# Optimization experiments

Hardware: AMD Instinct MI355X
Metric: run time of the kernel (lower is better)

The kernel has to match this reference:

```python
import jax, jax.numpy as jnp
import numpy as np

N, E, FDIM, HID, HEADS, C, L, G = 50000, 800000, 512, 256, 8, 32, 3, 64
EPS = 1e-5


def setup_inputs() -> dict:
    key = jax.random.key(0)
    ks = jax.random.split(key, 16)
    x = jax.random.normal(ks[0], (N, FDIM), dtype=jnp.float32)
    edge_index = jax.random.randint(ks[1], (2, E), 0, N, dtype=jnp.int32)
    batch = jnp.sort(jax.random.randint(ks[2], (N,), 0, G, dtype=jnp.int32))
    s = lambda f: 1.0 / np.sqrt(f)
    return {
        "x": x,
        "edge_index": edge_index,
        "batch": batch,
        "in_w": jax.random.normal(ks[3], (FDIM, HID), jnp.float32) * s(FDIM),
        "in_b": jnp.zeros((HID,), jnp.float32),
        "gat_w": jax.random.normal(ks[4], (L, HID, HID), jnp.float32) * s(HID),
        "att_src": jax.random.normal(ks[5], (L, HEADS, C), jnp.float32) * s(C),
        "att_dst": jax.random.normal(ks[6], (L, HEADS, C), jnp.float32) * s(C),
        "gat_b": jnp.zeros((L, HID), jnp.float32),
        "res_w": jax.random.normal(ks[7], (L, HID, HID), jnp.float32) * s(HID),
        "res_b": jnp.zeros((L, HID), jnp.float32),
        "ln_g": jnp.ones((L, HID), jnp.float32),
        "ln_b": jnp.zeros((L, HID), jnp.float32),
        "pool_w": jax.random.normal(ks[8], (2 * HID, HID), jnp.float32) * s(2 * HID),
        "pool_b": jnp.zeros((HID,), jnp.float32),
    }


def _gat_layer(h, src, dst, w, a_src, a_dst, b):
    # PyG GATConv, concat=True, negative_slope=0.2, dropout inactive (eval)
    xh = (h @ w).reshape(N, HEADS, C)                      # [N,H,C]
    asn = jnp.einsum('nhc,hc->nh', xh, a_src)              # [N,H]
    adn = jnp.einsum('nhc,hc->nh', xh, a_dst)
    e = jax.nn.leaky_relu(asn[src] + adn[dst], 0.2)        # [E2,H]
    # scatter-softmax over destination neighborhoods
    m = jax.ops.segment_max(e, dst, num_segments=N)
    m = jnp.where(jnp.isfinite(m), m, 0.0)
    ex = jnp.exp(e - m[dst])
    den = jax.ops.segment_sum(ex, dst, num_segments=N)
    alpha = ex / (den[dst] + 1e-16)                        # [E2,H]
    msg = xh[src] * alpha[:, :, None]                      # [E2,H,C]
    out = jax.ops.segment_sum(msg, dst, num_segments=N)    # [N,H,C]
    return out.reshape(N, HID) + b


def _layer_norm(h, g, b):
    mu = jnp.mean(h, axis=-1, keepdims=True)
    var = jnp.mean((h - mu) ** 2, axis=-1, keepdims=True)
    return (h - mu) * jax.lax.rsqrt(var + EPS) * g + b


def reference(x, edge_index, batch, in_w, in_b, gat_w, att_src, att_dst, gat_b,
              res_w, res_b, ln_g, ln_b, pool_w, pool_b):
    loops = jnp.arange(N, dtype=edge_index.dtype)          # GATConv add_self_loops=True
    src = jnp.concatenate([edge_index[0], loops])
    dst = jnp.concatenate([edge_index[1], loops])
    h = x @ in_w + in_b
    for i in range(L):
        h_res = h @ res_w[i] + res_b[i]
        h = _gat_layer(h, src, dst, gat_w[i], att_src[i], att_dst[i], gat_b[i])
        h = jax.nn.relu(_layer_norm(h + h_res, ln_g[i], ln_b[i]))
    ones = jnp.ones((N,), h.dtype)
    cnt = jax.ops.segment_sum(ones, batch, num_segments=G)
    h_mean = jax.ops.segment_sum(h, batch, num_segments=G) / jnp.maximum(cnt, 1.0)[:, None]
    h_max = jax.ops.segment_max(h, batch, num_segments=G)
    h_cat = jnp.concatenate([h_mean, h_max], axis=1)       # [G, 2*HID]
    return jax.nn.relu(h_cat @ pool_w + pool_b)            # [G, HID]
```

## Files before the change

### kernel.cpp

```cpp
#include <hip/hip_runtime.h>
#include <math.h>

#define N_NODES 50000
#define E_EDGES 800000
#define E2 (E_EDGES + N_NODES)
#define M_PAD 50048
#define NBM 391
#define GEMM_BLOCKS 1568
#define FDIM 512
#define HID 256
#define HEADS 8
#define CDIM 32
#define LAYERS 3
#define GRAPHS 64
#define LN_EPS 1e-5f
#define POOL_P 16

typedef unsigned short ushort_t;
typedef __attribute__((ext_vector_type(8))) short short8v;
typedef __attribute__((ext_vector_type(4))) float f32x4;

__device__ __forceinline__ float bf2f(ushort_t u) {
    union { unsigned int i; float f; } v;
    v.i = ((unsigned int)u) << 16;
    return v.f;
}
__device__ __forceinline__ ushort_t f2bf(float f) {
    union { float f; unsigned int u; } v;
    v.f = f;
    unsigned int r = (v.u + 0x7FFFu + ((v.u >> 16) & 1u)) >> 16;
    return (ushort_t)r;
}
__device__ __forceinline__ void gload_lds16(const void* g, void* l) {
    __builtin_amdgcn_global_load_lds(
        (const __attribute__((address_space(1))) void*)g,
        (__attribute__((address_space(3))) void*)l, 16, 0, 0);
}

__global__ void k_count(const int* __restrict__ ei, int* __restrict__ cnt) {
    int e = blockIdx.x * 256 + threadIdx.x;
    if (e >= E2) return;
    int dst = (e < E_EDGES) ? ei[E_EDGES + e] : (e - E_EDGES);
    atomicAdd(&cnt[dst], 1);
}

__global__ void k_scan1(const int* __restrict__ cnt, int* __restrict__ part) {
    __shared__ int s[256];
    int t = threadIdx.x;
    int i = blockIdx.x * 256 + t;
    s[t] = (i < N_NODES) ? cnt[i] : 0;
    __syncthreads();
    for (int d = 128; d > 0; d >>= 1) {
        if (t < d) s[t] += s[t + d];
        __syncthreads();
    }
    if (t == 0) part[blockIdx.x] = s[0];
}

__global__ void k_scan2(int* __restrict__ part, int nb, int* __restrict__ rowptr) {
    __shared__ int s[256];
    int t = threadIdx.x;
    int v = (t < nb) ? part[t] : 0;
    s[t] = v;
    __syncthreads();
    for (int d = 1; d < 256; d <<= 1) {
        int x = (t >= d) ? s[t - d] : 0;
        __syncthreads();
        s[t] += x;
        __syncthreads();
    }
    if (t < nb) part[t] = s[t] - v;
    if (t == 255) rowptr[N_NODES] = s[255];
}

__global__ void k_scan3(const int* __restrict__ cnt, const int* __restrict__ part,
                        int* __restrict__ rowptr) {
    __shared__ int s[256];
    int t = threadIdx.x;
    int i = blockIdx.x * 256 + t;
    int v = (i < N_NODES) ? cnt[i] : 0;
    s[t] = v;
    __syncthreads();
    for (int d = 1; d < 256; d <<= 1) {
        int x = (t >= d) ? s[t - d] : 0;
        __syncthreads();
        s[t] += x;
        __syncthreads();
    }
    if (i < N_NODES) rowptr[i] = part[blockIdx.x] + s[t] - v;
}

__global__ void k_fill(const int* __restrict__ ei, const int* __restrict__ rowptr,
                       int* __restrict__ fill, int* __restrict__ colv) {
    int e = blockIdx.x * 256 + threadIdx.x;
    if (e >= E2) return;
    int src, dst;
    if (e < E_EDGES) { src = ei[e]; dst = ei[E_EDGES + e]; }
    else             { src = dst = e - E_EDGES; }
    int pos = atomicAdd(&fill[dst], 1);
    colv[rowptr[dst] + pos] = src;
}

__global__ void k_bounds(const int* __restrict__ batch, int* __restrict__ rowstart) {
    int n = blockIdx.x * 256 + threadIdx.x;
    if (n >= N_NODES) return;
    int b = batch[n];
    int bp = (n == 0) ? -1 : batch[n - 1];
    for (int g = bp + 1; g <= b; ++g) rowstart[g] = n;
    if (n == N_NODES - 1) {
        for (int g = b + 1; g <= GRAPHS; ++g) rowstart[g] = N_NODES;
    }
}

__global__ __launch_bounds__(256) void k_cast_x(const float* __restrict__ x,
                                                ushort_t* __restrict__ xb) {
    long long i8 = ((long long)blockIdx.x * 256 + threadIdx.x) * 8;
    if (i8 >= (long long)M_PAD * FDIM) return;
    int row = (int)(i8 >> 9);
    ushort_t o[8];
    if (row < N_NODES) {
        const float* p = x + i8;
        #pragma unroll
        for (int j = 0; j < 8; ++j) o[j] = f2bf(p[j]);
    } else {
        #pragma unroll
        for (int j = 0; j < 8; ++j) o[j] = 0;
    }
    *(short8v*)(xb + i8) = *(short8v*)o;
}

#define MAT_ELEMS (HID * HID)
#define WT_TOTAL (2 * (LAYERS - 1) * MAT_ELEMS)
__global__ __launch_bounds__(256) void k_wtrans_all(const float* __restrict__ gat_w,
                                                    const float* __restrict__ res_w,
                                                    ushort_t* __restrict__ wt2) {
    int r = blockIdx.x * 256 + threadIdx.x;
    if (r >= WT_TOTAL) return;
    int mat = r >> 16;
    int layer = 1 + (mat >> 1);
    int isgat = mat & 1;
    int within = r & 65535;
    int k = within >> 8, n = within & 255;
    const float* W = (isgat ? gat_w : res_w) + (size_t)layer * MAT_ELEMS;
    wt2[(size_t)layer * 512 * HID + (size_t)(isgat * 256 + n) * HID + k] =
        f2bf(W[within]);
}

__global__ __launch_bounds__(256) void k_wcomb(const float* __restrict__ in_w,
                                               const float* __restrict__ in_b,
                                               const float* __restrict__ res_w0,
                                               const float* __restrict__ gat_w0,
                                               const float* __restrict__ res_b0,
                                               ushort_t* __restrict__ wtC,
                                               float* __restrict__ bC0,
                                               float* __restrict__ bC1) {
    if (blockIdx.x == 512) {
        int n = threadIdx.x;
        float s0 = 0.f, s1 = 0.f;
        for (int k = 0; k < HID; ++k) {
            float ib = in_b[k];
            s0 += ib * res_w0[(size_t)k * HID + n];
            s1 += ib * gat_w0[(size_t)k * HID + n];
        }
        bC0[n] = s0 + res_b0[n];
        bC1[n] = s1;
        return;
    }
    __shared__ float wrow[HID];
    int n = blockIdx.x;
    {
        int k = threadIdx.x;
        float wv = (n < 256) ? res_w0[(size_t)k * HID + n]
                             : gat_w0[(size_t)k * HID + (n - 256)];
        wrow[k] = bf2f(f2bf(wv));
    }
    __syncthreads();
    #pragma unroll
    for (int h = 0; h < 2; ++h) {
        int f = h * 256 + threadIdx.x;
        const float* irow = in_w + (size_t)f * HID;
        float s = 0.f;
        #pragma unroll 4
        for (int k = 0; k < HID; k += 4) {
            float4 iv = *(const float4*)(irow + k);
            s += iv.x * wrow[k] + iv.y * wrow[k + 1]
               + iv.z * wrow[k + 2] + iv.w * wrow[k + 3];
        }
        wtC[(size_t)n * FDIM + f] = f2bf(s);
    }
}

template<int K>
__global__ __launch_bounds__(512) void k_gemm_bf16(const ushort_t* __restrict__ A,
                                                   const ushort_t* __restrict__ BT,
                                                   const float* __restrict__ bias0,
                                                   const float* __restrict__ bias1,
                                                   ushort_t* __restrict__ C0,
                                                   ushort_t* __restrict__ C1,
                                                   const float* __restrict__ a_src,
                                                   const float* __restrict__ a_dst,
                                                   float* __restrict__ asn,
                                                   float* __restrict__ adn, int M) {
    const int L = blockIdx.x;
    const int chunk = L >> 5, wrd = L & 31;
    const int bmi = chunk * 8 + (wrd & 7);
    if (bmi >= NBM) return;
    const int bm = bmi * 128;
    const int bn = (wrd >> 3) * 128;

    __shared__ char lds[16384] __attribute__((aligned(16)));
    const int t = threadIdx.x, w = t >> 6, l = t & 63;
    const int wr = w & 3, wc = w >> 2;

    const int arow = t >> 2;
    const int aslot = (t & 3) ^ ((arow >> 1) & 3);
    const ushort_t* pa = A + (size_t)(bm + arow) * K + aslot * 8;
    const ushort_t* pb = BT + (size_t)(bn + arow) * K + aslot * 8;
    char* la = lds + w * 1024;
    char* lb = lds + 8192 + w * 1024;

    int aoff[2], boff[4];
    const int kb = l >> 4;
    #pragma unroll
    for (int mi = 0; mi < 2; ++mi) {
        int r = wr * 32 + mi * 16 + (l & 15);
        aoff[mi] = r * 64 + ((kb ^ ((r >> 1) & 3)) << 4);
    }
    #pragma unroll
    for (int ni = 0; ni < 4; ++ni) {
        int c = wc * 64 + ni * 16 + (l & 15);
        boff[ni] = 8192 + c * 64 + ((kb ^ ((c >> 1) & 3)) << 4);
    }

    f32x4 acc[2][4] = {};
    for (int k0 = 0; k0 < K; k0 += 32) {
        gload_lds16(pa + k0, la);
        gload_lds16(pb + k0, lb);
        __syncthreads();
        short8v a[2], b[4];
        #pragma unroll
        for (int mi = 0; mi < 2; ++mi) a[mi] = *(const short8v*)(lds + aoff[mi]);
        #pragma unroll
        for (int ni = 0; ni < 4; ++ni) b[ni] = *(const short8v*)(lds + boff[ni]);
        #pragma unroll
        for (int mi = 0; mi < 2; ++mi)
            #pragma unroll
            for (int ni = 0; ni < 4; ++ni)
                acc[mi][ni] = __builtin_amdgcn_mfma_f32_16x16x32_bf16(
                    a[mi], b[ni], acc[mi][ni], 0, 0, 0);
        __syncthreads();
    }

    ushort_t* C = (bn < 256) ? C0 : C1;
    const float* bias = (bn < 256) ? bias0 : bias1;
    const int cb = (bn < 256) ? bn : bn - 256;
    #pragma unroll
    for (int mi = 0; mi < 2; ++mi) {
        int row = bm + wr * 32 + mi * 16 + (l >> 4) * 4;
        #pragma unroll
        for (int ni = 0; ni < 4; ++ni) {
            int col = cb + wc * 64 + ni * 16 + (l & 15);
            float bv = bias ? bias[col] : 0.f;
            #pragma unroll
            for (int r = 0; r < 4; ++r) {
                if (row + r < M)
                    C[(size_t)(row + r) * HID + col] = f2bf(acc[mi][ni][r] + bv);
            }
        }
    }

    if (asn && bn >= 256) {
        const int cbase = bn - 256;
        #pragma unroll
        for (int mi = 0; mi < 2; ++mi) {
            int row = bm + wr * 32 + mi * 16 + (l >> 4) * 4;
            #pragma unroll
            for (int p = 0; p < 2; ++p) {
                int c0 = cbase + wc * 64 + (2 * p) * 16 + (l & 15);
                int c1c = c0 + 16;
                int head = c0 >> 5;
                float b1a = bias1 ? bias1[c0] : 0.f;
                float b1b = bias1 ? bias1[c1c] : 0.f;
                float as0 = a_src[c0], as1 = a_src[c1c];
                float ad0 = a_dst[c0], ad1 = a_dst[c1c];
                float vs[4], vd[4];
                #pragma unroll
                for (int r = 0; r < 4; ++r) {
                    float x0 = acc[mi][2 * p][r] + b1a;
                    float x1 = acc[mi][2 * p + 1][r] + b1b;
                    vs[r] = x0 * as0 + x1 * as1;
                    vd[r] = x0 * ad0 + x1 * ad1;
                }
                #pragma unroll
                for (int d = 1; d < 16; d <<= 1) {
                    #pragma unroll
                    for (int r = 0; r < 4; ++r) {
                        vs[r] += __shfl_xor(vs[r], d);
                        vd[r] += __shfl_xor(vd[r], d);
                    }
                }
                if ((l & 15) == 0) {
                    #pragma unroll
                    for (int r = 0; r < 4; ++r) {
                        if (row + r < N_NODES) {
                            asn[(row + r) * HEADS + head] = vs[r];
                            adn[(row + r) * HEADS + head] = vd[r];
                        }
                    }
                }
            }
        }
    }
}

__global__ __launch_bounds__(256) void k_agg_ln(const ushort_t* __restrict__ xhb,
                                                const float* __restrict__ asn,
                                                const float* __restrict__ adn,
                                                const int* __restrict__ rowptr,
                                                const int* __restrict__ colv,
                                                const ushort_t* __restrict__ hresb,
                                                const float* __restrict__ gb,
                                                const float* __restrict__ g,
                                                const float* __restrict__ b,
                                                ushort_t* __restrict__ hb) {
    const int wave = threadIdx.x >> 6, lane = threadIdx.x & 63;
    const int n = blockIdx.x * 4 + wave;
    if (n >= N_NODES) return;
    const int half = lane >> 5;
    const int lh = lane & 31;
    const int head = lh >> 2;
    const int ch0 = lh * 8;
    const float adn_h = adn[n * HEADS + head];
    const int j0 = rowptr[n], j1 = rowptr[n + 1];

    float acc[8] = {};
    float den = 0.f;
    int base = j0;
    for (; base + 8 <= j1; base += 8) {
        int idx[4];
        #pragma unroll
        for (int q = 0; q < 4; ++q) idx[q] = colv[base + 2 * q + half];
        short8v u[4];
        #pragma unroll
        for (int q = 0; q < 4; ++q)
            u[q] = *(const short8v*)(xhb + (size_t)idx[q] * HID + ch0);
        float p[4];
        #pragma unroll
        for (int q = 0; q < 4; ++q) {
            float e = asn[idx[q] * HEADS + head] + adn_h;
            e = (e > 0.f) ? e : 0.2f * e;
            p[q] = __expf(e);
        }
        #pragma unroll
        for (int q = 0; q < 4; ++q) {
            den += p[q];
            #pragma unroll
            for (int c = 0; c < 8; ++c)
                acc[c] += p[q] * bf2f((ushort_t)u[q][c]);
        }
    }
    for (; base < j1; base += 2) {
        bool valid = (base + half) < j1;
        int s = valid ? colv[base + half] : n;
        short8v u = *(const short8v*)(xhb + (size_t)s * HID + ch0);
        float e = asn[s * HEADS + head] + adn_h;
        e = (e > 0.f) ? e : 0.2f * e;
        float p = valid ? __expf(e) : 0.f;
        den += p;
        #pragma unroll
        for (int c = 0; c < 8; ++c)
            acc[c] += p * bf2f((ushort_t)u[c]);
    }
    den += __shfl_xor(den, 32);
    #pragma unroll
    for (int c = 0; c < 8; ++c) acc[c] += __shfl_xor(acc[c], 32);

    const float inv = 1.f / (den + 1e-16f);
    short8v hr = *(const short8v*)(hresb + (size_t)n * HID + ch0);
    float4 gbA = *(const float4*)(gb + ch0);
    float4 gbB = *(const float4*)(gb + ch0 + 4);
    float v[8];
    #pragma unroll
    for (int c = 0; c < 8; ++c) {
        float gbv = (c < 4) ? ((const float*)&gbA)[c] : ((const float*)&gbB)[c - 4];
        v[c] = acc[c] * inv + bf2f((ushort_t)hr[c]) + gbv;
    }
    float s = 0.f;
    #pragma unroll
    for (int c = 0; c < 8; ++c) s += v[c];
    #pragma unroll
    for (int d = 1; d < 32; d <<= 1) s += __shfl_xor(s, d);
    const float mu = s * (1.f / HID);
    float q = 0.f;
    #pragma unroll
    for (int c = 0; c < 8; ++c) {
        v[c] -= mu;
        q += v[c] * v[c];
    }
    #pragma unroll
    for (int d = 1; d < 32; d <<= 1) q += __shfl_xor(q, d);
    const float rstd = rsqrtf(q * (1.f / HID) + LN_EPS);
    float4 gA = *(const float4*)(g + ch0);
    float4 gB = *(const float4*)(g + ch0 + 4);
    float4 bA = *(const float4*)(b + ch0);
    float4 bB = *(const float4*)(b + ch0 + 4);
    ushort_t o[8];
    #pragma unroll
    for (int c = 0; c < 8; ++c) {
        float gv = (c < 4) ? ((const float*)&gA)[c] : ((const float*)&gB)[c - 4];
        float bv = (c < 4) ? ((const float*)&bA)[c] : ((const float*)&bB)[c - 4];
        o[c] = f2bf(fmaxf(v[c] * rstd * gv + bv, 0.f));
    }
    if (half == 0)
        *(short8v*)(hb + (size_t)n * HID + ch0) = *(short8v*)o;
}

__global__ __launch_bounds__(256) void k_pool1(const ushort_t* __restrict__ hb,
                                               const int* __restrict__ rowstart,
                                               float* __restrict__ part) {
    int g = blockIdx.x, p = blockIdx.y, c = threadIdx.x;
    int s0 = rowstart[g], s1 = rowstart[g + 1];
    float sum = 0.f, mx = -INFINITY;
    for (int n = s0 + p; n < s1; n += POOL_P) {
        float v = bf2f(hb[(size_t)n * HID + c]);
        sum += v;
        mx = fmaxf(mx, v);
    }
    float* pp = part + (size_t)(g * POOL_P + p) * 512;
    pp[c] = sum;
    pp[256 + c] = mx;
}

__global__ __launch_bounds__(256) void k_pool2g(const float* __restrict__ part,
                                                const int* __restrict__ rowstart,
                                                const float* __restrict__ W,
                                                const float* __restrict__ bias,
                                                float* __restrict__ out) {
    __shared__ float hc[512];
    int g = blockIdx.x, c = threadIdx.x;
    float sum = 0.f, mx = -INFINITY;
    for (int p = 0; p < POOL_P; ++p) {
        const float* pp = part + (size_t)(g * POOL_P + p) * 512;
        sum += pp[c];
        mx = fmaxf(mx, pp[256 + c]);
    }
    float cntf = (float)(rowstart[g + 1] - rowstart[g]);
    hc[c] = sum / fmaxf(cntf, 1.f);
    hc[256 + c] = mx;
    __syncthreads();
    float acc = bias[c];
    #pragma unroll 8
    for (int k = 0; k < 2 * HID; ++k)
        acc += hc[k] * W[(size_t)k * HID + c];
    out[(size_t)g * HID + c] = fmaxf(acc, 0.f);
}

extern "C" void kernel_launch(void* const* d_in, const int* in_sizes, int n_in,
                              void* d_out, int out_size, void* d_ws, size_t ws_size,
                              hipStream_t stream) {
    const float* x       = (const float*)d_in[0];
    const int*   ei      = (const int*)d_in[1];
    const int*   batch   = (const int*)d_in[2];
    const float* in_w    = (const float*)d_in[3];
    const float* in_b    = (const float*)d_in[4];
    const float* gat_w   = (const float*)d_in[5];
    const float* att_src = (const float*)d_in[6];
    const float* att_dst = (const float*)d_in[7];
    const float* gat_b   = (const float*)d_in[8];
    const float* res_w   = (const float*)d_in[9];
    const float* res_b   = (const float*)d_in[10];
    const float* ln_g    = (const float*)d_in[11];
    const float* ln_b    = (const float*)d_in[12];
    const float* pool_w  = (const float*)d_in[13];
    const float* pool_b  = (const float*)d_in[14];
    float* out = (float*)d_out;

    char* ws = (char*)d_ws;
    size_t off = 0;
    auto alloc = [&](size_t bytes) -> char* {
        char* p = ws + off;
        off = (off + bytes + 255) & ~(size_t)255;
        return p;
    };
    ushort_t* xb    = (ushort_t*)alloc((size_t)M_PAD * FDIM * 2);
    ushort_t* hb    = (ushort_t*)alloc((size_t)M_PAD * HID * 2);
    ushort_t* xhb   = (ushort_t*)alloc((size_t)M_PAD * HID * 2);
    ushort_t* hresb = (ushort_t*)alloc((size_t)M_PAD * HID * 2);
    float* asn      = (float*)alloc((size_t)N_NODES * HEADS * 4);
    float* adn      = (float*)alloc((size_t)N_NODES * HEADS * 4);
    int*   cnt      = (int*)alloc((size_t)N_NODES * 4);
    int*   fill     = (int*)alloc((size_t)N_NODES * 4);
    int*   rowptr   = (int*)alloc((size_t)(N_NODES + 1) * 4);
    int*   colv     = (int*)alloc((size_t)E2 * 4);
    int*   part     = (int*)alloc(256 * 4);
    int*   rowstart = (int*)alloc((size_t)(GRAPHS + 1) * 4);
    ushort_t* wt2   = (ushort_t*)alloc((size_t)LAYERS * 512 * HID * 2);
    ushort_t* wtC   = (ushort_t*)alloc((size_t)512 * FDIM * 2);
    float* bC0      = (float*)alloc(HID * 4);
    float* bC1      = (float*)alloc(HID * 4);
    float* poolpart = (float*)alloc((size_t)GRAPHS * POOL_P * 512 * 4);

    hipMemsetAsync(cnt, 0, (size_t)N_NODES * 4, stream);
    hipMemsetAsync(fill, 0, (size_t)N_NODES * 4, stream);

    const int ge = (E2 + 255) / 256;
    const int nb = (N_NODES + 255) / 256;
    k_count<<<ge, 256, 0, stream>>>(ei, cnt);
    k_scan1<<<nb, 256, 0, stream>>>(cnt, part);
    k_scan2<<<1, 256, 0, stream>>>(part, nb, rowptr);
    k_scan3<<<nb, 256, 0, stream>>>(cnt, part, rowptr);
    k_fill<<<ge, 256, 0, stream>>>(ei, rowptr, fill, colv);
    k_bounds<<<nb, 256, 0, stream>>>(batch, rowstart);

    k_cast_x<<<(int)(((size_t)M_PAD * FDIM / 8 + 255) / 256), 256, 0, stream>>>(x, xb);
    k_wtrans_all<<<(WT_TOTAL + 255) / 256, 256, 0, stream>>>(gat_w, res_w, wt2);
    k_wcomb<<<513, 256, 0, stream>>>(in_w, in_b, res_w, gat_w, res_b,
                                     wtC, bC0, bC1);

    const int nw = (N_NODES + 3) / 4;

    k_gemm_bf16<FDIM><<<GEMM_BLOCKS, 512, 0, stream>>>(xb, wtC, bC0, bC1,
                                                       hresb, xhb, att_src, att_dst,
                                                       asn, adn, N_NODES);
    k_agg_ln<<<nw, 256, 0, stream>>>(xhb, asn, adn, rowptr, colv, hresb,
                                     gat_b, ln_g, ln_b, hb);

    for (int i = 1; i < LAYERS; ++i) {
        k_gemm_bf16<HID><<<GEMM_BLOCKS, 512, 0, stream>>>(
            hb, wt2 + (size_t)i * 512 * HID,
            res_b + (size_t)i * HID, nullptr, hresb, xhb,
            att_src + (size_t)i * HEADS * CDIM,
            att_dst + (size_t)i * HEADS * CDIM, asn, adn, N_NODES);
        k_agg_ln<<<nw, 256, 0, stream>>>(xhb, asn, adn, rowptr, colv, hresb,
                                         gat_b + (size_t)i * HID,
                                         ln_g + (size_t)i * HID,
                                         ln_b + (size_t)i * HID, hb);
    }
    dim3 pg(GRAPHS, POOL_P);
    k_pool1<<<pg, 256, 0, stream>>>(hb, rowstart, poolpart);
    k_pool2g<<<GRAPHS, 256, 0, stream>>>(poolpart, rowstart, pool_w, pool_b, out);
}
```

Measured before the change: 570.3 us.

## Fuse fp32-to-bf16 cast of x into first GEMM and merge prep kernels

Removes the separate x cast kernel and its bf16 buffer. The first GEMM now loads fp32 rows of x straight into LDS, using a doubled A tile with an XOR swizzle, and converts them to bf16 in registers with v_cvt_pk_bf16_f32. The edge count, batch bounds, weight transpose and combined-weight kernels are merged into a single k_prep launch, which cuts launch overhead. In exchange the first GEMM reads twice the A bytes and uses more LDS per block, and out-of-range rows are clamped to row 0.

```diff
diff --git a/kernel.cpp b/kernel.cpp
--- a/kernel.cpp
+++ b/kernel.cpp
@@ -37,13 +37,6 @@
         (__attribute__((address_space(3))) void*)l, 16, 0, 0);
 }
 
-__global__ void k_count(const int* __restrict__ ei, int* __restrict__ cnt) {
-    int e = blockIdx.x * 256 + threadIdx.x;
-    if (e >= E2) return;
-    int dst = (e < E_EDGES) ? ei[E_EDGES + e] : (e - E_EDGES);
-    atomicAdd(&cnt[dst], 1);
-}
-
 __global__ void k_scan1(const int* __restrict__ cnt, int* __restrict__ part) {
     __shared__ int s[256];
     int t = threadIdx.x;
@@ -101,60 +94,63 @@
     colv[rowptr[dst] + pos] = src;
 }
 
-__global__ void k_bounds(const int* __restrict__ batch, int* __restrict__ rowstart) {
-    int n = blockIdx.x * 256 + threadIdx.x;
-    if (n >= N_NODES) return;
-    int b = batch[n];
-    int bp = (n == 0) ? -1 : batch[n - 1];
-    for (int g = bp + 1; g <= b; ++g) rowstart[g] = n;
-    if (n == N_NODES - 1) {
-        for (int g = b + 1; g <= GRAPHS; ++g) rowstart[g] = N_NODES;
-    }
-}
-
-__global__ __launch_bounds__(256) void k_cast_x(const float* __restrict__ x,
-                                                ushort_t* __restrict__ xb) {
-    long long i8 = ((long long)blockIdx.x * 256 + threadIdx.x) * 8;
-    if (i8 >= (long long)M_PAD * FDIM) return;
-    int row = (int)(i8 >> 9);
-    ushort_t o[8];
-    if (row < N_NODES) {
-        const float* p = x + i8;
-        #pragma unroll
-        for (int j = 0; j < 8; ++j) o[j] = f2bf(p[j]);
-    } else {
-        #pragma unroll
-        for (int j = 0; j < 8; ++j) o[j] = 0;
-    }
-    *(short8v*)(xb + i8) = *(short8v*)o;
-}
-
+#define GE_BLK ((E2 + 255) / 256)
+#define NB_BLK ((N_NODES + 255) / 256)
 #define MAT_ELEMS (HID * HID)
 #define WT_TOTAL (2 * (LAYERS - 1) * MAT_ELEMS)
-__global__ __launch_bounds__(256) void k_wtrans_all(const float* __restrict__ gat_w,
-                                                    const float* __restrict__ res_w,
-                                                    ushort_t* __restrict__ wt2) {
-    int r = blockIdx.x * 256 + threadIdx.x;
-    if (r >= WT_TOTAL) return;
-    int mat = r >> 16;
-    int layer = 1 + (mat >> 1);
-    int isgat = mat & 1;
-    int within = r & 65535;
-    int k = within >> 8, n = within & 255;
-    const float* W = (isgat ? gat_w : res_w) + (size_t)layer * MAT_ELEMS;
-    wt2[(size_t)layer * 512 * HID + (size_t)(isgat * 256 + n) * HID + k] =
-        f2bf(W[within]);
-}
-
-__global__ __launch_bounds__(256) void k_wcomb(const float* __restrict__ in_w,
-                                               const float* __restrict__ in_b,
-                                               const float* __restrict__ res_w0,
-                                               const float* __restrict__ gat_w0,
-                                               const float* __restrict__ res_b0,
-                                               ushort_t* __restrict__ wtC,
-                                               float* __restrict__ bC0,
-                                               float* __restrict__ bC1) {
-    if (blockIdx.x == 512) {
+#define WT_BLK (WT_TOTAL / 256)
+#define PREP_BLOCKS (GE_BLK + NB_BLK + WT_BLK + 513)
+
+__global__ __launch_bounds__(256) void k_prep(const int* __restrict__ ei,
+                                              const int* __restrict__ batch,
+                                              const float* __restrict__ in_w,
+                                              const float* __restrict__ in_b,
+                                              const float* __restrict__ gat_w,
+                                              const float* __restrict__ res_w,
+                                              const float* __restrict__ res_b,
+                                              int* __restrict__ cnt,
+                                              int* __restrict__ rowstart,
+                                              ushort_t* __restrict__ wt2,
+                                              ushort_t* __restrict__ wtC,
+                                              float* __restrict__ bC0,
+                                              float* __restrict__ bC1) {
+    int bid = blockIdx.x;
+    if (bid < GE_BLK) {
+        int e = bid * 256 + threadIdx.x;
+        if (e >= E2) return;
+        int dst = (e < E_EDGES) ? ei[E_EDGES + e] : (e - E_EDGES);
+        atomicAdd(&cnt[dst], 1);
+        return;
+    }
+    bid -= GE_BLK;
+    if (bid < NB_BLK) {
+        int n = bid * 256 + threadIdx.x;
+        if (n >= N_NODES) return;
+        int b = batch[n];
+        int bp = (n == 0) ? -1 : batch[n - 1];
+        for (int g = bp + 1; g <= b; ++g) rowstart[g] = n;
+        if (n == N_NODES - 1) {
+            for (int g = b + 1; g <= GRAPHS; ++g) rowstart[g] = N_NODES;
+        }
+        return;
+    }
+    bid -= NB_BLK;
+    if (bid < WT_BLK) {
+        int r = bid * 256 + threadIdx.x;
+        int mat = r >> 16;
+        int layer = 1 + (mat >> 1);
+        int isgat = mat & 1;
+        int within = r & 65535;
+        int k = within >> 8, n = within & 255;
+        const float* W = (isgat ? gat_w : res_w) + (size_t)layer * MAT_ELEMS;
+        wt2[(size_t)layer * 512 * HID + (size_t)(isgat * 256 + n) * HID + k] =
+            f2bf(W[within]);
+        return;
+    }
+    bid -= WT_BLK;
+    const float* res_w0 = res_w;
+    const float* gat_w0 = gat_w;
+    if (bid == 512) {
         int n = threadIdx.x;
         float s0 = 0.f, s1 = 0.f;
         for (int k = 0; k < HID; ++k) {
@@ -162,12 +158,12 @@
             s0 += ib * res_w0[(size_t)k * HID + n];
             s1 += ib * gat_w0[(size_t)k * HID + n];
         }
-        bC0[n] = s0 + res_b0[n];
+        bC0[n] = s0 + res_b[n];
         bC1[n] = s1;
         return;
     }
     __shared__ float wrow[HID];
-    int n = blockIdx.x;
+    int n = bid;
     {
         int k = threadIdx.x;
         float wv = (n < 256) ? res_w0[(size_t)k * HID + n]
@@ -190,8 +186,8 @@
     }
 }
 
-template<int K>
-__global__ __launch_bounds__(512) void k_gemm_bf16(const ushort_t* __restrict__ A,
+template<int K, bool AFP32>
+__global__ __launch_bounds__(512) void k_gemm_bf16(const void* __restrict__ Av,
                                                    const ushort_t* __restrict__ BT,
                                                    const float* __restrict__ bias0,
                                                    const float* __restrict__ bias1,
@@ -208,38 +204,78 @@
     const int bm = bmi * 128;
     const int bn = (wrd >> 3) * 128;
 
-    __shared__ char lds[16384] __attribute__((aligned(16)));
+    constexpr int ABYTES = AFP32 ? 16384 : 8192;
+    __shared__ char lds[ABYTES + 8192] __attribute__((aligned(16)));
     const int t = threadIdx.x, w = t >> 6, l = t & 63;
     const int wr = w & 3, wc = w >> 2;
 
-    const int arow = t >> 2;
-    const int aslot = (t & 3) ^ ((arow >> 1) & 3);
-    const ushort_t* pa = A + (size_t)(bm + arow) * K + aslot * 8;
-    const ushort_t* pb = BT + (size_t)(bn + arow) * K + aslot * 8;
-    char* la = lds + w * 1024;
-    char* lb = lds + 8192 + w * 1024;
-
-    int aoff[2], boff[4];
+    const int brow = t >> 2;
+    const int bslot = (t & 3) ^ ((brow >> 1) & 3);
+    const ushort_t* pb = BT + (size_t)(bn + brow) * K + bslot * 8;
+    char* lb = lds + ABYTES + w * 1024;
+
+    const ushort_t* pa = nullptr;
+    const float* paf1 = nullptr;
+    const float* paf2 = nullptr;
+    if constexpr (AFP32) {
+        const int c2 = t + 512;
+        const int ar1 = t >> 3,  as1 = (t & 7) ^ (ar1 & 7);
+        const int ar2 = c2 >> 3, as2 = (c2 & 7) ^ (ar2 & 7);
+        int gr1 = bm + ar1; if (gr1 >= M) gr1 = 0;
+        int gr2 = bm + ar2; if (gr2 >= M) gr2 = 0;
+        paf1 = (const float*)Av + (size_t)gr1 * K + as1 * 4;
+        paf2 = (const float*)Av + (size_t)gr2 * K + as2 * 4;
+    } else {
+        pa = (const ushort_t*)Av + (size_t)(bm + brow) * K + bslot * 8;
+    }
+
     const int kb = l >> 4;
+    int aoff[2];
+    int aoffF[2][2];
+    int boff[4];
     #pragma unroll
     for (int mi = 0; mi < 2; ++mi) {
         int r = wr * 32 + mi * 16 + (l & 15);
-        aoff[mi] = r * 64 + ((kb ^ ((r >> 1) & 3)) << 4);
+        if constexpr (AFP32) {
+            #pragma unroll
+            for (int j = 0; j < 2; ++j)
+                aoffF[mi][j] = r * 128 + (((2 * kb + j) ^ (r & 7)) << 4);
+        } else {
+            aoff[mi] = r * 64 + ((kb ^ ((r >> 1) & 3)) << 4);
+        }
     }
     #pragma unroll
     for (int ni = 0; ni < 4; ++ni) {
         int c = wc * 64 + ni * 16 + (l & 15);
-        boff[ni] = 8192 + c * 64 + ((kb ^ ((c >> 1) & 3)) << 4);
+        boff[ni] = ABYTES + c * 64 + ((kb ^ ((c >> 1) & 3)) << 4);
     }
 
     f32x4 acc[2][4] = {};
     for (int k0 = 0; k0 < K; k0 += 32) {
-        gload_lds16(pa + k0, la);
+        if constexpr (AFP32) {
+            gload_lds16(paf1 + k0, lds + w * 1024);
+            gload_lds16(paf2 + k0, lds + 8192 + w * 1024);
+        } else {
+            gload_lds16(pa + k0, lds + w * 1024);
+        }
         gload_lds16(pb + k0, lb);
         __syncthreads();
         short8v a[2], b[4];
         #pragma unroll
-        for (int mi = 0; mi < 2; ++mi) a[mi] = *(const short8v*)(lds + aoff[mi]);
+        for (int mi = 0; mi < 2; ++mi) {
+            if constexpr (AFP32) {
+                f32x4 f0 = *(const f32x4*)(lds + aoffF[mi][0]);
+                f32x4 f1 = *(const f32x4*)(lds + aoffF[mi][1]);
+                union { unsigned int u[4]; short8v s; } cv;
+                asm("v_cvt_pk_bf16_f32 %0, %1, %2" : "=v"(cv.u[0]) : "v"(f0[0]), "v"(f0[1]));
+                asm("v_cvt_pk_bf16_f32 %0, %1, %2" : "=v"(cv.u[1]) : "v"(f0[2]), "v"(f0[3]));
+                asm("v_cvt_pk_bf16_f32 %0, %1, %2" : "=v"(cv.u[2]) : "v"(f1[0]), "v"(f1[1]));
+                asm("v_cvt_pk_bf16_f32 %0, %1, %2" : "=v"(cv.u[3]) : "v"(f1[2]), "v"(f1[3]));
+                a[mi] = cv.s;
+            } else {
+                a[mi] = *(const short8v*)(lds + aoff[mi]);
+            }
+        }
         #pragma unroll
         for (int ni = 0; ni < 4; ++ni) b[ni] = *(const short8v*)(lds + boff[ni]);
         #pragma unroll
@@ -482,7 +518,6 @@
         off = (off + bytes + 255) & ~(size_t)255;
         return p;
     };
-    ushort_t* xb    = (ushort_t*)alloc((size_t)M_PAD * FDIM * 2);
     ushort_t* hb    = (ushort_t*)alloc((size_t)M_PAD * HID * 2);
     ushort_t* xhb   = (ushort_t*)alloc((size_t)M_PAD * HID * 2);
     ushort_t* hresb = (ushort_t*)alloc((size_t)M_PAD * HID * 2);
@@ -503,31 +538,27 @@
     hipMemsetAsync(cnt, 0, (size_t)N_NODES * 4, stream);
     hipMemsetAsync(fill, 0, (size_t)N_NODES * 4, stream);
 
-    const int ge = (E2 + 255) / 256;
-    const int nb = (N_NODES + 255) / 256;
-    k_count<<<ge, 256, 0, stream>>>(ei, cnt);
+    const int ge = GE_BLK;
+    const int nb = NB_BLK;
+    k_prep<<<PREP_BLOCKS, 256, 0, stream>>>(ei, batch, in_w, in_b, gat_w, res_w,
+                                            res_b, cnt, rowstart, wt2, wtC,
+                                            bC0, bC1);
     k_scan1<<<nb, 256, 0, stream>>>(cnt, part);
     k_scan2<<<1, 256, 0, stream>>>(part, nb, rowptr);
     k_scan3<<<nb, 256, 0, stream>>>(cnt, part, rowptr);
     k_fill<<<ge, 256, 0, stream>>>(ei, rowptr, fill, colv);
-    k_bounds<<<nb, 256, 0, stream>>>(batch, rowstart);
-
-    k_cast_x<<<(int)(((size_t)M_PAD * FDIM / 8 + 255) / 256), 256, 0, stream>>>(x, xb);
-    k_wtrans_all<<<(WT_TOTAL + 255) / 256, 256, 0, stream>>>(gat_w, res_w, wt2);
-    k_wcomb<<<513, 256, 0, stream>>>(in_w, in_b, res_w, gat_w, res_b,
-                                     wtC, bC0, bC1);
 
     const int nw = (N_NODES + 3) / 4;
 
-    k_gemm_bf16<FDIM><<<GEMM_BLOCKS, 512, 0, stream>>>(xb, wtC, bC0, bC1,
-                                                       hresb, xhb, att_src, att_dst,
-                                                       asn, adn, N_NODES);
+    k_gemm_bf16<FDIM, true><<<GEMM_BLOCKS, 512, 0, stream>>>(
+        (const void*)x, wtC, bC0, bC1, hresb, xhb, att_src, att_dst,
+        asn, adn, N_NODES);
     k_agg_ln<<<nw, 256, 0, stream>>>(xhb, asn, adn, rowptr, colv, hresb,
                                      gat_b, ln_g, ln_b, hb);
 
     for (int i = 1; i < LAYERS; ++i) {
-        k_gemm_bf16<HID><<<GEMM_BLOCKS, 512, 0, stream>>>(
-            hb, wt2 + (size_t)i * 512 * HID,
+        k_gemm_bf16<HID, false><<<GEMM_BLOCKS, 512, 0, stream>>>(
+            (const void*)hb, wt2 + (size_t)i * 512 * HID,
             res_b + (size_t)i * HID, nullptr, hresb, xhb,
             att_src + (size_t)i * HEADS * CDIM,
             att_dst + (size_t)i * HEADS * CDIM, asn, adn, N_NODES);
```

Result: slower. 596.9 us (+4.7%).
